# Performance work log

Hardware: AMD Instinct MI355X
Metric: run time of the kernel (lower is better)

The kernel has to match this reference:

```python
import jax, jax.numpy as jnp
import numpy as np

N = 50000      # nodes
E = 800000     # edges (before self loops)
F_IN = 128     # num_features
D = 128        # d_graph_layer
L = 3          # n_graph_layer (extra GAT layers after conv1)
DFC = 128      # d_FC_layer
NFC = 2        # n_FC_layer
C = 2          # num_classes
G = 1000       # number of graphs
NEG_SLOPE = 0.2


def setup_inputs() -> dict:
    key = jax.random.key(0)
    ks = jax.random.split(key, 24)
    s = lambda d: 1.0 / np.sqrt(d)
    inp = {
        "x": jax.random.normal(ks[0], (N, F_IN), jnp.float32),
        "energy": jax.random.normal(ks[1], (G, 1), jnp.float32),
        # conv1 params
        "W1": jax.random.normal(ks[2], (F_IN, D), jnp.float32) * s(F_IN),
        "as1": jax.random.normal(ks[3], (D,), jnp.float32) * s(D),
        "ad1": jax.random.normal(ks[4], (D,), jnp.float32) * s(D),
        "b1": jnp.zeros((D,), jnp.float32),
        # stacked convs params
        "Ws": jax.random.normal(ks[5], (L, D, D), jnp.float32) * s(D),
        "ass": jax.random.normal(ks[6], (L, D), jnp.float32) * s(D),
        "ads": jax.random.normal(ks[7], (L, D), jnp.float32) * s(D),
        "bs": jnp.zeros((L, D), jnp.float32),
        # FC head
        "lin0_W": jax.random.normal(ks[8], (D, DFC), jnp.float32) * s(D),
        "lin0_b": jnp.zeros((DFC,), jnp.float32),
        "lin1_W": jax.random.normal(ks[9], (DFC + 1, DFC), jnp.float32) * s(DFC + 1),
        "lin1_b": jnp.zeros((DFC,), jnp.float32),
        "lins_W": jax.random.normal(ks[10], (NFC - 1, DFC, DFC), jnp.float32) * s(DFC),
        "lins_b": jnp.zeros((NFC - 1, DFC), jnp.float32),
        "lin3_W": jax.random.normal(ks[11], (DFC, C), jnp.float32) * s(DFC),
        "lin3_b": jnp.zeros((C,), jnp.float32),
        # graph structure
        "edge_index": jax.random.randint(ks[12], (2, E), 0, N, dtype=jnp.int64),
        "batchs": jnp.sort(jax.random.randint(ks[13], (N,), 0, G, dtype=jnp.int64)),
    }
    return inp


def gat_layer(x, W, a_src, a_dst, b, src, dst):
    # GATConv (heads=1): h = xW; e_ij = LeakyReLU(a_src.h_src + a_dst.h_dst);
    # alpha = softmax over edges grouped by dst; out_i = sum alpha * h_src + b
    h = x @ W                                        # [N, D]
    e = jax.nn.leaky_relu((h @ a_src)[src] + (h @ a_dst)[dst], NEG_SLOPE)  # [E']
    m = jax.ops.segment_max(e, dst, num_segments=N)  # every node has a self loop
    w = jnp.exp(e - m[dst])
    denom = jax.ops.segment_sum(w, dst, num_segments=N)
    alpha = w / denom[dst]
    out = jax.ops.segment_sum(h[src] * alpha[:, None], dst, num_segments=N)
    return out + b


def reference(x, energy, W1, as1, ad1, b1, Ws, ass, ads, bs,
              lin0_W, lin0_b, lin1_W, lin1_b, lins_W, lins_b,
              lin3_W, lin3_b, edge_index, batchs):
    loop = jnp.arange(N, dtype=edge_index.dtype)     # GATConv add_self_loops
    src = jnp.concatenate([edge_index[0], loop])
    dst = jnp.concatenate([edge_index[1], loop])

    h = jax.nn.relu(gat_layer(x, W1, as1, ad1, b1, src, dst))
    for i in range(L):
        h = jax.nn.relu(gat_layer(h, Ws[i], ass[i], ads[i], bs[i], src, dst))

    g = jax.ops.segment_sum(h, batchs, num_segments=G)   # global_add_pool [G, D]
    y = jax.nn.relu(g @ lin0_W + lin0_b)                 # lins[0]
    z = jax.nn.relu(jnp.concatenate([y, energy], axis=1) @ lin1_W + lin1_b)
    z = z + y                                            # residual
    for i in range(NFC - 1):
        z = jax.nn.relu(z @ lins_W[i] + lins_b[i])
    logits = z @ lin3_W + lin3_b
    return jax.nn.log_softmax(logits, axis=1)            # last == 'log'
```

## Files before the change

kernel.cpp:

```cpp
#include <hip/hip_runtime.h>
#include <math.h>

#define NN 50000
#define EE 800000
#define ET 850000
#define DD 128
#define GG 1000
#define SLOPE 0.2f

#define KB   2048
#define NBA  416
#define BSZ  4096
#define NBUK 208

typedef unsigned int  u32;
typedef unsigned short u16;

__device__ __forceinline__ u16 f2h(float f){
  return __builtin_bit_cast(unsigned short, (_Float16)f);
}
__device__ __forceinline__ float hlo(u32 d){
  return (float)__builtin_bit_cast(_Float16, (unsigned short)(d & 0xFFFFu));
}
__device__ __forceinline__ float hhi(u32 d){
  return (float)__builtin_bit_cast(_Float16, (unsigned short)(d >> 16));
}

__global__ void init_k(const int* __restrict__ batchs, int* __restrict__ cnt,
                       int* __restrict__ gstart, int* __restrict__ bcur){
  int n = blockIdx.x*256 + threadIdx.x;
  if (n < NBUK) bcur[n] = 0;
  if (n < NN){
    cnt[n] = 0;
    int b = batchs[n];
    int prev = n ? batchs[n-1] : -1;
    for (int g = prev+1; g <= b; ++g) gstart[g] = n;
    if (n == NN-1){
      for (int g = b+1; g <= GG; ++g) gstart[g] = NN;
    }
  }
}

__global__ void count_k(const int* __restrict__ ei, int* __restrict__ cnt,
                        int* __restrict__ rank){
  int e = blockIdx.x*256 + threadIdx.x;
  if (e < ET){
    int d = (e < EE) ? ei[EE + e] : (e - EE);
    rank[e] = atomicAdd(&cnt[d], 1);
  }
}

__global__ __launch_bounds__(256) void blocksum_k(const int* __restrict__ cnt,
                                                  int* __restrict__ bsum){
  int i = blockIdx.x*256 + threadIdx.x;
  int v = (i < NN) ? cnt[i] : 0;
  #pragma unroll
  for (int o=32;o;o>>=1) v += __shfl_xor(v,o);
  __shared__ int ws[4];
  if ((threadIdx.x & 63) == 0) ws[threadIdx.x>>6] = v;
  __syncthreads();
  if (threadIdx.x == 0) bsum[blockIdx.x] = ws[0]+ws[1]+ws[2]+ws[3];
}

__global__ __launch_bounds__(256) void scanb_k(int* __restrict__ bsum, int nb){
  int tid = threadIdx.x;
  int v = (tid < nb) ? bsum[tid] : 0;
  int lane = tid & 63, wv = tid >> 6;
  int s = v;
  #pragma unroll
  for (int o=1;o<64;o<<=1){ int t = __shfl_up(s,o); if (lane>=o) s += t; }
  __shared__ int ws[4];
  if (lane == 63) ws[wv] = s;
  __syncthreads();
  int woff = 0;
  for (int k=0;k<wv;++k) woff += ws[k];
  if (tid < nb) bsum[tid] = s - v + woff;
}

__global__ __launch_bounds__(256) void scatter_k(const int* __restrict__ cnt,
                                                 const int* __restrict__ bsum,
                                                 int* __restrict__ row_start){
  int i = blockIdx.x*256 + threadIdx.x;
  int v = (i < NN) ? cnt[i] : 0;
  int lane = threadIdx.x & 63, wv = threadIdx.x >> 6;
  int s = v;
  #pragma unroll
  for (int o=1;o<64;o<<=1){ int t = __shfl_up(s,o); if (lane>=o) s += t; }
  __shared__ int ws[4];
  if (lane == 63) ws[wv] = s;
  __syncthreads();
  int woff = 0;
  for (int k=0;k<wv;++k) woff += ws[k];
  int off = s - v + woff + bsum[blockIdx.x];
  if (i < NN) row_start[i] = off;
  if (i == 0) row_start[NN] = ET;
}

__global__ __launch_bounds__(256) void partA_k(const int* __restrict__ ei,
                                               const int* __restrict__ rank,
                                               const int* __restrict__ row_start,
                                               int* __restrict__ bcur,
                                               uint2* __restrict__ stage){
  __shared__ uint2 lpairs[KB];
  __shared__ int lcnt[256], lstart[256], lrun[256], gbase[256];
  __shared__ int ws[4];
  int tid = threadIdx.x;
  int base = blockIdx.x * KB;
  int nE = min(KB, ET - base);
  lcnt[tid] = 0;
  __syncthreads();
  u32 pos_r[KB/256]; u32 src_r[KB/256];
  #pragma unroll
  for (int i=0;i<KB/256;++i){
    int e = base + i*256 + tid;
    u32 p = 0xFFFFFFFFu, s = 0;
    if (e < ET){
      int d, sr;
      if (e < EE){ sr = ei[e]; d = ei[EE + e]; }
      else       { sr = e - EE; d = sr; }
      p = (u32)(row_start[d] + rank[e]);
      s = (u32)sr;
      atomicAdd(&lcnt[p >> 12], 1);
    }
    pos_r[i] = p; src_r[i] = s;
  }
  __syncthreads();
  int v = lcnt[tid];
  int lane = tid & 63, wv = tid >> 6;
  int s = v;
  #pragma unroll
  for (int o=1;o<64;o<<=1){ int t = __shfl_up(s,o); if (lane>=o) s += t; }
  if (lane == 63) ws[wv] = s;
  __syncthreads();
  int woff = 0;
  for (int k=0;k<wv;++k) woff += ws[k];
  int excl = s - v + woff;
  lstart[tid] = excl;
  lrun[tid]   = excl;
  gbase[tid]  = (tid < NBUK && v > 0) ? atomicAdd(&bcur[tid], v) : 0;
  __syncthreads();
  #pragma unroll
  for (int i=0;i<KB/256;++i){
    if (pos_r[i] != 0xFFFFFFFFu){
      int b = pos_r[i] >> 12;
      int slot = atomicAdd(&lrun[b], 1);
      lpairs[slot] = make_uint2(pos_r[i], src_r[i]);
    }
  }
  __syncthreads();
  for (int j = tid; j < nE; j += 256){
    uint2 pr = lpairs[j];
    int b = pr.x >> 12;
    int dest = (b << 12) + gbase[b] + (j - lstart[b]);
    stage[dest] = pr;
  }
}

__global__ __launch_bounds__(256) void partB_k(const uint2* __restrict__ stage,
                                               int* __restrict__ srcs){
  __shared__ int buf[BSZ];
  int b = blockIdx.x, tid = threadIdx.x;
  int base = b << 12;
  int n_b = min(BSZ, ET - base);
  for (int j = tid; j < n_b; j += 256){
    uint2 pr = stage[base + j];
    buf[pr.x - base] = (int)pr.y;
  }
  __syncthreads();
  for (int j = tid; j*4 < n_b; j += 256){
    *(int4*)(srcs + base + j*4) = *(const int4*)(buf + j*4);
  }
}

__global__ __launch_bounds__(256) void gemm_rb_k(const float* __restrict__ A,
                                                 const float* __restrict__ W,
                                                 const float* __restrict__ as,
                                                 const float* __restrict__ ad,
                                                 u16* __restrict__ Ch,
                                                 float* __restrict__ hs,
                                                 float* __restrict__ hd){
  __shared__ float As[2][16][68];
  __shared__ float Wsh[2][16][128];
  int tid = threadIdx.x;
  int rbase = blockIdx.x*64;
  int ty = tid >> 4, tx = tid & 15;
  int arow = tid >> 2, aq = tid & 3;
  int wk = tid >> 5, wc = tid & 31;

  float4 aReg, w0Reg, w1Reg;
  {
    int r = rbase + arow;
    aReg = (r < NN) ? *(const float4*)(A + (size_t)r*DD + aq*4) : float4{0,0,0,0};
    w0Reg = *(const float4*)(W + (size_t)wk*DD + wc*4);
    w1Reg = *(const float4*)(W + (size_t)(wk+8)*DD + wc*4);
  }
  As[0][aq*4+0][arow] = aReg.x;
  As[0][aq*4+1][arow] = aReg.y;
  As[0][aq*4+2][arow] = aReg.z;
  As[0][aq*4+3][arow] = aReg.w;
  *(float4*)(&Wsh[0][wk][wc*4])   = w0Reg;
  *(float4*)(&Wsh[0][wk+8][wc*4]) = w1Reg;
  __syncthreads();

  float acc[4][8] = {};
  for (int t=0; t<8; ++t){
    int cur = t & 1;
    if (t < 7){
      int k0 = (t+1)*16;
      int r = rbase + arow;
      aReg = (r < NN) ? *(const float4*)(A + (size_t)r*DD + k0 + aq*4) : float4{0,0,0,0};
      w0Reg = *(const float4*)(W + (size_t)(k0+wk)*DD + wc*4);
      w1Reg = *(const float4*)(W + (size_t)(k0+wk+8)*DD + wc*4);
    }
    #pragma unroll
    for (int k=0;k<16;++k){
      float4 a4  = *(const float4*)(&As[cur][k][ty*4]);
      float4 wA  = *(const float4*)(&Wsh[cur][k][tx*8]);
      float4 wB  = *(const float4*)(&Wsh[cur][k][tx*8+4]);
      float a[4] = {a4.x, a4.y, a4.z, a4.w};
      float wv[8] = {wA.x, wA.y, wA.z, wA.w, wB.x, wB.y, wB.z, wB.w};
      #pragma unroll
      for (int ii=0;ii<4;++ii)
        #pragma unroll
        for (int jj=0;jj<8;++jj)
          acc[ii][jj] += a[ii]*wv[jj];
    }
    if (t < 7){
      __syncthreads();
      int nxt = cur ^ 1;
      As[nxt][aq*4+0][arow] = aReg.x;
      As[nxt][aq*4+1][arow] = aReg.y;
      As[nxt][aq*4+2][arow] = aReg.z;
      As[nxt][aq*4+3][arow] = aReg.w;
      *(float4*)(&Wsh[nxt][wk][wc*4])   = w0Reg;
      *(float4*)(&Wsh[nxt][wk+8][wc*4]) = w1Reg;
      __syncthreads();
    }
  }

  float4 s0 = *(const float4*)(as + tx*8);
  float4 s1 = *(const float4*)(as + tx*8 + 4);
  float4 d0 = *(const float4*)(ad + tx*8);
  float4 d1 = *(const float4*)(ad + tx*8 + 4);
  #pragma unroll
  for (int ii=0;ii<4;++ii){
    float ds = acc[ii][0]*s0.x + acc[ii][1]*s0.y + acc[ii][2]*s0.z + acc[ii][3]*s0.w
             + acc[ii][4]*s1.x + acc[ii][5]*s1.y + acc[ii][6]*s1.z + acc[ii][7]*s1.w;
    float dd = acc[ii][0]*d0.x + acc[ii][1]*d0.y + acc[ii][2]*d0.z + acc[ii][3]*d0.w
             + acc[ii][4]*d1.x + acc[ii][5]*d1.y + acc[ii][6]*d1.z + acc[ii][7]*d1.w;
    #pragma unroll
    for (int o=1;o<16;o<<=1){ ds += __shfl_xor(ds,o); dd += __shfl_xor(dd,o); }
    int r = rbase + ty*4 + ii;
    if (tx == 0 && r < NN){ hs[r] = ds; hd[r] = dd; }
  }
  #pragma unroll
  for (int ii=0;ii<4;++ii){
    int r = rbase + ty*4 + ii;
    if (r < NN){
      ushort4 o0 = {f2h(acc[ii][0]), f2h(acc[ii][1]), f2h(acc[ii][2]), f2h(acc[ii][3])};
      ushort4 o1 = {f2h(acc[ii][4]), f2h(acc[ii][5]), f2h(acc[ii][6]), f2h(acc[ii][7])};
      *(ushort4*)(Ch + (size_t)r*DD + tx*8)     = o0;
      *(ushort4*)(Ch + (size_t)r*DD + tx*8 + 4) = o1;
    }
  }
}

__global__ __launch_bounds__(256) void gat_agg_h_k(const u16* __restrict__ hh,
                                                   const float* __restrict__ hs,
                                                   const float* __restrict__ hd,
                                                   const int* __restrict__ row_start,
                                                   const int* __restrict__ srcs,
                                                   const float* __restrict__ bias,
                                                   float* __restrict__ out){
  int node = blockIdx.x*4 + (threadIdx.x >> 6);
  int lane = threadIdx.x & 63;
  if (node >= NN) return;
  int half = lane >> 5;
  int hl   = lane & 31;
  int beg = row_start[node], end = row_start[node+1];
  float hdn = hd[node];
  float m = -INFINITY, denom = 0.f;
  float a0=0.f, a1=0.f, a2=0.f, a3=0.f;
  for (int c=beg; c<end; c+=64){
    int nc = min(64, end-c);
    float e = -INFINITY; int src = 0;
    if (lane < nc){
      src = srcs[c+lane];
      float t = hs[src] + hdn;
      e = (t >= 0.f) ? t : SLOPE*t;
    }
    float cm = e;
    #pragma unroll
    for (int o=32;o;o>>=1) cm = fmaxf(cm, __shfl_xor(cm,o));
    float nm = fmaxf(m, cm);
    float w = (lane < nc) ? expf(e - nm) : 0.f;
    float cs = w;
    #pragma unroll
    for (int o=32;o;o>>=1) cs += __shfl_xor(cs,o);
    float scale = expf(m - nm);
    denom = denom*scale + cs;
    a0 *= scale; a1 *= scale; a2 *= scale; a3 *= scale;
    m = nm;
    int nh = (nc + 1 - half) >> 1;
    for (int i=0;i<nh;++i){
      int j = 2*i + half;
      float wi = __shfl(w, j);
      int   si = __shfl(src, j);
      uint2 hv = *(const uint2*)(hh + (size_t)si*DD + hl*4);
      a0 += wi*hlo(hv.x); a1 += wi*hhi(hv.x);
      a2 += wi*hlo(hv.y); a3 += wi*hhi(hv.y);
    }
  }
  a0 += __shfl_xor(a0, 32);
  a1 += __shfl_xor(a1, 32);
  a2 += __shfl_xor(a2, 32);
  a3 += __shfl_xor(a3, 32);
  if (half == 0){
    float inv = 1.f/denom;
    float4 b4 = *(const float4*)(bias + hl*4);
    float4 o4;
    o4.x = fmaxf(a0*inv + b4.x, 0.f);
    o4.y = fmaxf(a1*inv + b4.y, 0.f);
    o4.z = fmaxf(a2*inv + b4.z, 0.f);
    o4.w = fmaxf(a3*inv + b4.w, 0.f);
    *(float4*)(out + (size_t)node*DD + hl*4) = o4;
  }
}

__global__ __launch_bounds__(128) void tail_k(const float* __restrict__ h,
                                              const int* __restrict__ gstart,
                                              const float* __restrict__ energy,
                                              const float* __restrict__ W0, const float* __restrict__ b0,
                                              const float* __restrict__ W1, const float* __restrict__ b1,
                                              const float* __restrict__ W2, const float* __restrict__ b2,
                                              const float* __restrict__ W3, const float* __restrict__ b3,
                                              float* __restrict__ out){
  __shared__ float row[DD];
  __shared__ float buf[DD];
  int gr = blockIdx.x, j = threadIdx.x;
  int beg = gstart[gr], end = gstart[gr+1];
  float s = 0.f;
  for (int n=beg; n<end; ++n) s += h[(size_t)n*DD + j];
  row[j] = s;
  __syncthreads();
  float acc = 0.f;
  #pragma unroll 8
  for (int k=0;k<DD;++k) acc += row[k]*W0[k*DD + j];
  float y = fmaxf(acc + b0[j], 0.f);
  buf[j] = y;
  __syncthreads();
  acc = 0.f;
  #pragma unroll 8
  for (int k=0;k<DD;++k) acc += buf[k]*W1[k*DD + j];
  acc += energy[gr]*W1[DD*DD + j];
  float z = fmaxf(acc + b1[j], 0.f) + y;
  __syncthreads();
  row[j] = z;
  __syncthreads();
  acc = 0.f;
  #pragma unroll 8
  for (int k=0;k<DD;++k) acc += row[k]*W2[k*DD + j];
  float z2 = fmaxf(acc + b2[j], 0.f);
  buf[j] = z2;
  __syncthreads();
  if (j < 64){
    float za = buf[j], zb = buf[j+64];
    float l0 = za*W3[j*2]     + zb*W3[(j+64)*2];
    float l1 = za*W3[j*2 + 1] + zb*W3[(j+64)*2 + 1];
    #pragma unroll
    for (int o=32;o;o>>=1){ l0 += __shfl_xor(l0,o); l1 += __shfl_xor(l1,o); }
    if (j == 0){
      l0 += b3[0]; l1 += b3[1];
      float mx = fmaxf(l0, l1);
      float lse = mx + logf(expf(l0-mx) + expf(l1-mx));
      out[gr*2]   = l0 - lse;
      out[gr*2+1] = l1 - lse;
    }
  }
}

extern "C" void kernel_launch(void* const* d_in, const int* in_sizes, int n_in,
                              void* d_out, int out_size, void* d_ws, size_t ws_size,
                              hipStream_t stream) {
  const float* x      = (const float*)d_in[0];
  const float* energy = (const float*)d_in[1];
  const float* W1     = (const float*)d_in[2];
  const float* as1    = (const float*)d_in[3];
  const float* ad1    = (const float*)d_in[4];
  const float* b1     = (const float*)d_in[5];
  const float* Ws     = (const float*)d_in[6];
  const float* ass    = (const float*)d_in[7];
  const float* ads    = (const float*)d_in[8];
  const float* bs     = (const float*)d_in[9];
  const float* lin0_W = (const float*)d_in[10];
  const float* lin0_b = (const float*)d_in[11];
  const float* lin1_W = (const float*)d_in[12];
  const float* lin1_b = (const float*)d_in[13];
  const float* lins_W = (const float*)d_in[14];
  const float* lins_b = (const float*)d_in[15];
  const float* lin3_W = (const float*)d_in[16];
  const float* lin3_b = (const float*)d_in[17];
  const int*   ei     = (const int*)d_in[18];
  const int*   batchs = (const int*)d_in[19];
  float* out = (float*)d_out;

  char* wp = (char*)d_ws;
  auto alloc = [&](size_t bytes)->void*{
    void* p = (void*)wp;
    wp += (bytes + 255) & ~(size_t)255;
    return p;
  };
  float* hA        = (float*)alloc((size_t)NN*DD*4);
  float* hB        = (float*)alloc((size_t)NN*DD*4);
  u16*   hHf       = (u16*)hB;
  float* hs        = (float*)alloc((size_t)NN*4);
  float* hd        = (float*)alloc((size_t)NN*4);
  int*   cnt       = (int*)alloc((size_t)NN*4);
  int*   row_start = (int*)alloc((size_t)(NN+1)*4);
  int*   rank      = (int*)alloc((size_t)ET*4);
  int*   srcs      = (int*)alloc((size_t)ET*4);
  uint2* stage     = (uint2*)alloc((size_t)NBUK*BSZ*8);
  int*   bcur      = (int*)alloc((size_t)NBUK*4);
  int*   gstart    = (int*)alloc((size_t)(GG+1)*4);
  int*   bsum      = (int*)alloc((size_t)256*4);

  const int NB_N  = (NN + 255)/256;
  const int NB_E  = (ET + 255)/256;
  const int NB_W  = (NN + 3)/4;
  const int NB_G  = (NN + 63)/64;

  init_k<<<NB_N, 256, 0, stream>>>(batchs, cnt, gstart, bcur);
  count_k<<<NB_E, 256, 0, stream>>>(ei, cnt, rank);
  blocksum_k<<<NB_N, 256, 0, stream>>>(cnt, bsum);
  scanb_k<<<1, 256, 0, stream>>>(bsum, NB_N);
  scatter_k<<<NB_N, 256, 0, stream>>>(cnt, bsum, row_start);
  partA_k<<<NBA, 256, 0, stream>>>(ei, rank, row_start, bcur, stage);
  partB_k<<<NBUK, 256, 0, stream>>>(stage, srcs);

  gemm_rb_k<<<NB_G, 256, 0, stream>>>(x, W1, as1, ad1, hHf, hs, hd);
  gat_agg_h_k<<<NB_W, 256, 0, stream>>>(hHf, hs, hd, row_start, srcs, b1, hA);
  for (int l=1; l<4; ++l){
    const float* Wl  = Ws  + (size_t)(l-1)*DD*DD;
    const float* asl = ass + (size_t)(l-1)*DD;
    const float* adl = ads + (size_t)(l-1)*DD;
    const float* bl  = bs  + (size_t)(l-1)*DD;
    gemm_rb_k<<<NB_G, 256, 0, stream>>>(hA, Wl, asl, adl, hHf, hs, hd);
    gat_agg_h_k<<<NB_W, 256, 0, stream>>>(hHf, hs, hd, row_start, srcs, bl, hA);
  }

  tail_k<<<GG, 128, 0, stream>>>(hA, gstart, energy,
                                 lin0_W, lin0_b, lin1_W, lin1_b,
                                 lins_W, lins_b, lin3_W, lin3_b, out);
}
```

Baseline: 525.2 us.

## Replace FP32 register-blocked GEMM with FP16 MFMA matrix-core GEMM

```diff
diff --git a/kernel.cpp b/kernel.cpp
--- a/kernel.cpp
+++ b/kernel.cpp
@@ -13,8 +13,13 @@
 #define BSZ  4096
 #define NBUK 208
 
+#define LSTR 136
+
 typedef unsigned int  u32;
 typedef unsigned short u16;
+typedef _Float16 f16;
+typedef __attribute__((ext_vector_type(8))) _Float16 f16x8;
+typedef __attribute__((ext_vector_type(4))) float f32x4;
 
 __device__ __forceinline__ u16 f2h(float f){
   return __builtin_bit_cast(unsigned short, (_Float16)f);
@@ -172,95 +177,92 @@
   }
 }
 
-__global__ __launch_bounds__(256) void gemm_rb_k(const float* __restrict__ A,
-                                                 const float* __restrict__ W,
-                                                 const float* __restrict__ as,
-                                                 const float* __restrict__ ad,
-                                                 u16* __restrict__ Ch,
-                                                 float* __restrict__ hs,
-                                                 float* __restrict__ hd){
-  __shared__ float As[2][16][68];
-  __shared__ float Wsh[2][16][128];
+__global__ __launch_bounds__(256) void gemm_mfma_k(const float* __restrict__ A,
+                                                   const float* __restrict__ W,
+                                                   const float* __restrict__ as,
+                                                   const float* __restrict__ ad,
+                                                   u16* __restrict__ Ch,
+                                                   float* __restrict__ hs,
+                                                   float* __restrict__ hd){
+  __shared__ u16 Al[64*LSTR];
+  __shared__ u16 Wt[128*LSTR];
   int tid = threadIdx.x;
   int rbase = blockIdx.x*64;
-  int ty = tid >> 4, tx = tid & 15;
-  int arow = tid >> 2, aq = tid & 3;
-  int wk = tid >> 5, wc = tid & 31;
-
-  float4 aReg, w0Reg, w1Reg;
-  {
-    int r = rbase + arow;
-    aReg = (r < NN) ? *(const float4*)(A + (size_t)r*DD + aq*4) : float4{0,0,0,0};
-    w0Reg = *(const float4*)(W + (size_t)wk*DD + wc*4);
-    w1Reg = *(const float4*)(W + (size_t)(wk+8)*DD + wc*4);
-  }
-  As[0][aq*4+0][arow] = aReg.x;
-  As[0][aq*4+1][arow] = aReg.y;
-  As[0][aq*4+2][arow] = aReg.z;
-  As[0][aq*4+3][arow] = aReg.w;
-  *(float4*)(&Wsh[0][wk][wc*4])   = w0Reg;
-  *(float4*)(&Wsh[0][wk+8][wc*4]) = w1Reg;
-  __syncthreads();
-
-  float acc[4][8] = {};
-  for (int t=0; t<8; ++t){
-    int cur = t & 1;
-    if (t < 7){
-      int k0 = (t+1)*16;
-      int r = rbase + arow;
-      aReg = (r < NN) ? *(const float4*)(A + (size_t)r*DD + k0 + aq*4) : float4{0,0,0,0};
-      w0Reg = *(const float4*)(W + (size_t)(k0+wk)*DD + wc*4);
-      w1Reg = *(const float4*)(W + (size_t)(k0+wk+8)*DD + wc*4);
-    }
-    #pragma unroll
-    for (int k=0;k<16;++k){
-      float4 a4  = *(const float4*)(&As[cur][k][ty*4]);
-      float4 wA  = *(const float4*)(&Wsh[cur][k][tx*8]);
-      float4 wB  = *(const float4*)(&Wsh[cur][k][tx*8+4]);
-      float a[4] = {a4.x, a4.y, a4.z, a4.w};
-      float wv[8] = {wA.x, wA.y, wA.z, wA.w, wB.x, wB.y, wB.z, wB.w};
+
+  #pragma unroll
+  for (int it=0; it<8; ++it){
+    int i = it*256 + tid;
+    int r = i >> 5, c4 = i & 31;
+    float4 v = {0.f,0.f,0.f,0.f};
+    if (rbase + r < NN) v = *(const float4*)(A + (size_t)(rbase+r)*DD + c4*4);
+    u32 p0 = (u32)f2h(v.x) | ((u32)f2h(v.y) << 16);
+    u32 p1 = (u32)f2h(v.z) | ((u32)f2h(v.w) << 16);
+    *(u32*)(&Al[r*LSTR + c4*4])     = p0;
+    *(u32*)(&Al[r*LSTR + c4*4 + 2]) = p1;
+  }
+  #pragma unroll
+  for (int it=0; it<16; ++it){
+    int i = it*256 + tid;
+    int k = i >> 5, c4 = i & 31;
+    float4 v = *(const float4*)(W + (size_t)k*DD + c4*4);
+    Wt[(c4*4+0)*LSTR + k] = f2h(v.x);
+    Wt[(c4*4+1)*LSTR + k] = f2h(v.y);
+    Wt[(c4*4+2)*LSTR + k] = f2h(v.z);
+    Wt[(c4*4+3)*LSTR + k] = f2h(v.w);
+  }
+  __syncthreads();
+
+  int wid = tid >> 6;
+  int l   = tid & 63;
+  int lr  = l & 15;
+  int lk  = l >> 4;
+
+  f32x4 acc[8] = {};
+  #pragma unroll
+  for (int ks=0; ks<4; ++ks){
+    int k0 = ks*32;
+    f16x8 a = *(const f16x8*)(&Al[(wid*16+lr)*LSTR + k0 + lk*8]);
+    #pragma unroll
+    for (int ct=0; ct<8; ++ct){
+      f16x8 b = *(const f16x8*)(&Wt[(ct*16+lr)*LSTR + k0 + lk*8]);
+      acc[ct] = __builtin_amdgcn_mfma_f32_16x16x32_f16(a, b, acc[ct], 0, 0, 0);
+    }
+  }
+
+  float hsum[4] = {0.f,0.f,0.f,0.f};
+  float hdsum[4] = {0.f,0.f,0.f,0.f};
+  #pragma unroll
+  for (int ct=0; ct<8; ++ct){
+    float a_s = as[ct*16 + lr];
+    float a_d = ad[ct*16 + lr];
+    #pragma unroll
+    for (int i=0;i<4;++i){
+      hsum[i]  += acc[ct][i]*a_s;
+      hdsum[i] += acc[ct][i]*a_d;
+    }
+  }
+  #pragma unroll
+  for (int i=0;i<4;++i){
+    #pragma unroll
+    for (int o=1;o<16;o<<=1){
+      hsum[i]  += __shfl_xor(hsum[i],  o);
+      hdsum[i] += __shfl_xor(hdsum[i], o);
+    }
+  }
+  if (lr == 0){
+    #pragma unroll
+    for (int i=0;i<4;++i){
+      int r = rbase + wid*16 + lk*4 + i;
+      if (r < NN){ hs[r] = hsum[i]; hd[r] = hdsum[i]; }
+    }
+  }
+  #pragma unroll
+  for (int i=0;i<4;++i){
+    int r = rbase + wid*16 + lk*4 + i;
+    if (r < NN){
       #pragma unroll
-      for (int ii=0;ii<4;++ii)
-        #pragma unroll
-        for (int jj=0;jj<8;++jj)
-          acc[ii][jj] += a[ii]*wv[jj];
-    }
-    if (t < 7){
-      __syncthreads();
-      int nxt = cur ^ 1;
-      As[nxt][aq*4+0][arow] = aReg.x;
-      As[nxt][aq*4+1][arow] = aReg.y;
-      As[nxt][aq*4+2][arow] = aReg.z;
-      As[nxt][aq*4+3][arow] = aReg.w;
-      *(float4*)(&Wsh[nxt][wk][wc*4])   = w0Reg;
-      *(float4*)(&Wsh[nxt][wk+8][wc*4]) = w1Reg;
-      __syncthreads();
-    }
-  }
-
-  float4 s0 = *(const float4*)(as + tx*8);
-  float4 s1 = *(const float4*)(as + tx*8 + 4);
-  float4 d0 = *(const float4*)(ad + tx*8);
-  float4 d1 = *(const float4*)(ad + tx*8 + 4);
-  #pragma unroll
-  for (int ii=0;ii<4;++ii){
-    float ds = acc[ii][0]*s0.x + acc[ii][1]*s0.y + acc[ii][2]*s0.z + acc[ii][3]*s0.w
-             + acc[ii][4]*s1.x + acc[ii][5]*s1.y + acc[ii][6]*s1.z + acc[ii][7]*s1.w;
-    float dd = acc[ii][0]*d0.x + acc[ii][1]*d0.y + acc[ii][2]*d0.z + acc[ii][3]*d0.w
-             + acc[ii][4]*d1.x + acc[ii][5]*d1.y + acc[ii][6]*d1.z + acc[ii][7]*d1.w;
-    #pragma unroll
-    for (int o=1;o<16;o<<=1){ ds += __shfl_xor(ds,o); dd += __shfl_xor(dd,o); }
-    int r = rbase + ty*4 + ii;
-    if (tx == 0 && r < NN){ hs[r] = ds; hd[r] = dd; }
-  }
-  #pragma unroll
-  for (int ii=0;ii<4;++ii){
-    int r = rbase + ty*4 + ii;
-    if (r < NN){
-      ushort4 o0 = {f2h(acc[ii][0]), f2h(acc[ii][1]), f2h(acc[ii][2]), f2h(acc[ii][3])};
-      ushort4 o1 = {f2h(acc[ii][4]), f2h(acc[ii][5]), f2h(acc[ii][6]), f2h(acc[ii][7])};
-      *(ushort4*)(Ch + (size_t)r*DD + tx*8)     = o0;
-      *(ushort4*)(Ch + (size_t)r*DD + tx*8 + 4) = o1;
+      for (int ct=0; ct<8; ++ct)
+        Ch[(size_t)r*DD + ct*16 + lr] = f2h(acc[ct][i]);
     }
   }
 }
@@ -437,14 +439,14 @@
   partA_k<<<NBA, 256, 0, stream>>>(ei, rank, row_start, bcur, stage);
   partB_k<<<NBUK, 256, 0, stream>>>(stage, srcs);
 
-  gemm_rb_k<<<NB_G, 256, 0, stream>>>(x, W1, as1, ad1, hHf, hs, hd);
+  gemm_mfma_k<<<NB_G, 256, 0, stream>>>(x, W1, as1, ad1, hHf, hs, hd);
   gat_agg_h_k<<<NB_W, 256, 0, stream>>>(hHf, hs, hd, row_start, srcs, b1, hA);
   for (int l=1; l<4; ++l){
     const float* Wl  = Ws  + (size_t)(l-1)*DD*DD;
     const float* asl = ass + (size_t)(l-1)*DD;
     const float* adl = ads + (size_t)(l-1)*DD;
     const float* bl  = bs  + (size_t)(l-1)*DD;
-    gemm_rb_k<<<NB_G, 256, 0, stream>>>(hA, Wl, asl, adl, hHf, hs, hd);
+    gemm_mfma_k<<<NB_G, 256, 0, stream>>>(hA, Wl, asl, adl, hHf, hs, hd);
     gat_agg_h_k<<<NB_W, 256, 0, stream>>>(hHf, hs, hd, row_start, srcs, bl, hA);
   }
 
```

Result: faster. 481.8 us (-8.3%).
